# Optimization experiments

Measured on AMD Instinct MI355X. Metric: run time of the kernel, lower is better.

The kernel has to match this reference:

```python
import jax, jax.numpy as jnp
import numpy as np

B, D, H, E, C = 16384, 1024, 2048, 8, 3


def setup_inputs() -> dict:
    key = jax.random.key(0)
    ks = jax.random.split(key, 5)
    s_in = 1.0 / np.sqrt(D)
    s_h = 1.0 / np.sqrt(H)
    return {
        "x": jax.random.normal(ks[0], (B, D), dtype=jnp.float32),
        "Wr": jax.random.normal(ks[1], (D, E), dtype=jnp.float32) * s_in,
        "br": jnp.zeros((E,), dtype=jnp.float32),
        "W1": jax.random.normal(ks[2], (E, D, H), dtype=jnp.float32) * s_in,
        "b1": jnp.zeros((E, H), dtype=jnp.float32),
        "W2": jax.random.normal(ks[3], (E, H, C), dtype=jnp.float32) * s_h,
        "b2": jnp.zeros((E, C), dtype=jnp.float32),
    }


def reference(x, Wr, br, W1, b1, W2, b2):
    # Router: hard top-1 topic assignment per row.  [B]
    topics = jnp.argmax(x @ Wr + br, axis=1)
    # Dense dispatch: run every expert on all tokens (jit-friendly equivalent
    # of the masked per-expert loop), then combine by selecting the routed
    # expert's output per row.
    h = jax.nn.relu(jnp.einsum("bd,edh->ebh", x, W1) + b1[:, None, :])  # [E,B,H]
    out_all = jnp.einsum("ebh,ehc->ebc", h, W2) + b2[:, None, :]        # [E,B,C]
    preds = out_all[topics, jnp.arange(x.shape[0])]                     # [B,C]
    return preds
```

## Files before the change

kernel.cpp:

```cpp
#include <hip/hip_runtime.h>
#include <hip/hip_bf16.h>
#include <stdint.h>

#define NB 16384
#define ND 1024
#define NH 2048
#define NE 8
#define NC 3
#define MAXWL 136

typedef __attribute__((ext_vector_type(8))) short short8;
typedef __attribute__((ext_vector_type(4))) short short4v;
typedef __attribute__((ext_vector_type(4))) float f32x4;

__device__ __forceinline__ unsigned short f2bf(float f) {
  union { float f; unsigned int u; } v; v.f = f;
  unsigned int u = v.u;
  return (unsigned short)((u + 0x7fffu + ((u >> 16) & 1u)) >> 16);
}

__device__ __forceinline__ void glds16(const void* g, void* l) {
  __builtin_amdgcn_global_load_lds(
      (const __attribute__((address_space(1))) void*)g,
      (__attribute__((address_space(3))) void*)l,
      16, 0, 0);
}

__global__ __launch_bounds__(256) void router_kernel(
    const float* __restrict__ x, const float* __restrict__ Wr,
    const float* __restrict__ br, unsigned short* __restrict__ xb,
    int* __restrict__ topics) {
  int w = threadIdx.x >> 6, lane = threadIdx.x & 63;
  int row0 = blockIdx.x * 16 + w * 4;
  const float* xr[4];
  unsigned short* xbr[4];
#pragma unroll
  for (int r = 0; r < 4; ++r) {
    xr[r] = x + (size_t)(row0 + r) * ND;
    xbr[r] = xb + (size_t)(row0 + r) * ND;
  }
  f32x4 xv[4][4];
#pragma unroll
  for (int r = 0; r < 4; ++r)
#pragma unroll
    for (int i = 0; i < 4; ++i)
      xv[r][i] = *(const f32x4*)(xr[r] + i * 256 + lane * 4);
  float p[4][NE];
#pragma unroll
  for (int r = 0; r < 4; ++r)
#pragma unroll
    for (int e = 0; e < NE; ++e) p[r][e] = 0.f;
#pragma unroll
  for (int i = 0; i < 4; ++i) {
    int k0 = i * 256 + lane * 4;
#pragma unroll
    for (int r = 0; r < 4; ++r) {
      short4v s;
#pragma unroll
      for (int j = 0; j < 4; ++j) s[j] = (short)f2bf(xv[r][i][j]);
      *(short4v*)(xbr[r] + k0) = s;
    }
#pragma unroll
    for (int j = 0; j < 4; ++j) {
      const f32x4* wp = (const f32x4*)(Wr + (size_t)(k0 + j) * NE);
      f32x4 wa = wp[0], wb = wp[1];
#pragma unroll
      for (int r = 0; r < 4; ++r) {
        float a = xv[r][i][j];
        p[r][0] = fmaf(a, wa[0], p[r][0]);
        p[r][1] = fmaf(a, wa[1], p[r][1]);
        p[r][2] = fmaf(a, wa[2], p[r][2]);
        p[r][3] = fmaf(a, wa[3], p[r][3]);
        p[r][4] = fmaf(a, wb[0], p[r][4]);
        p[r][5] = fmaf(a, wb[1], p[r][5]);
        p[r][6] = fmaf(a, wb[2], p[r][6]);
        p[r][7] = fmaf(a, wb[3], p[r][7]);
      }
    }
  }
#pragma unroll
  for (int r = 0; r < 4; ++r)
#pragma unroll
    for (int e = 0; e < NE; ++e) {
#pragma unroll
      for (int d = 1; d < 64; d <<= 1) p[r][e] += __shfl_xor(p[r][e], d);
    }
  if (lane == 0) {
#pragma unroll
    for (int r = 0; r < 4; ++r) {
      float best = -1e30f;
      int bi = 0;
#pragma unroll
      for (int e = 0; e < NE; ++e) {
        float v = p[r][e] + br[e];
        if (v > best) { best = v; bi = e; }
      }
      topics[row0 + r] = bi;
    }
  }
}

__global__ __launch_bounds__(1024) void ranker_w1t_kernel(
    const int* __restrict__ topics, const float* __restrict__ W1,
    unsigned short* __restrict__ w1t, int* __restrict__ perm,
    int* __restrict__ counts, int* __restrict__ offsets,
    int* __restrict__ worklist, int* __restrict__ n_wl) {
  __shared__ __align__(16) char smem[8 * 64 * 67 * 2];
  __shared__ int soff[NE];
  int tid = threadIdx.x;

  if (blockIdx.x < 512) {
    unsigned short(*sbuf_t)[64][67] = (unsigned short(*)[64][67])smem;
    int bid = blockIdx.x;
    int e = bid >> 6;
    int rem = bid & 63;
    int kb = rem >> 2;
    int hb0 = (rem & 3) * 8;
    int kl = tid >> 4;
    int h0 = (tid & 15) * 4;
    const float* src = W1 + ((size_t)e * ND + kb * 64) * NH + hb0 * 64;
    f32x4 v[8];
#pragma unroll
    for (int q = 0; q < 8; ++q)
      v[q] = *(const f32x4*)(src + (size_t)kl * NH + q * 64 + h0);
#pragma unroll
    for (int q = 0; q < 8; ++q) {
#pragma unroll
      for (int j = 0; j < 4; ++j) sbuf_t[q][kl][h0 + j] = f2bf(v[q][j]);
    }
    __syncthreads();
#pragma unroll
    for (int s = 0; s < 4; ++s) {
      int flat = s * 1024 + tid;
      int q = flat >> 9;
      int idx = flat & 511;
      int hl = idx >> 3;
      int c8 = (idx & 7) * 8;
      short8 sv;
#pragma unroll
      for (int j = 0; j < 8; ++j) sv[j] = (short)sbuf_t[q][c8 + j][hl];
      unsigned short* dst =
          w1t + ((size_t)e * NH + (hb0 + q) * 64 + hl) * ND + kb * 64 + c8;
      *(short8*)dst = sv;
    }
    return;
  }

  uint4* sbuf = (uint4*)smem;
  int t[16];
  const int4* tp = (const int4*)(topics + tid * 16);
#pragma unroll
  for (int i = 0; i < 4; ++i) {
    int4 v = tp[i];
    t[i * 4 + 0] = v.x; t[i * 4 + 1] = v.y;
    t[i * 4 + 2] = v.z; t[i * 4 + 3] = v.w;
  }
  int h[NE] = {0, 0, 0, 0, 0, 0, 0, 0};
#pragma unroll
  for (int i = 0; i < 16; ++i) {
#pragma unroll
    for (int q = 0; q < NE; ++q) h[q] += (t[i] == q);
  }
  uint4 pk;
  pk.x = (unsigned)h[0] | ((unsigned)h[1] << 16);
  pk.y = (unsigned)h[2] | ((unsigned)h[3] << 16);
  pk.z = (unsigned)h[4] | ((unsigned)h[5] << 16);
  pk.w = (unsigned)h[6] | ((unsigned)h[7] << 16);
  uint4 own = pk;
  sbuf[tid] = pk;
  __syncthreads();
  for (int d = 1; d < 1024; d <<= 1) {
    uint4 v = {0u, 0u, 0u, 0u};
    if (tid >= d) v = sbuf[tid - d];
    __syncthreads();
    pk.x += v.x; pk.y += v.y; pk.z += v.z; pk.w += v.w;
    sbuf[tid] = pk;
    __syncthreads();
  }
  if (tid == 0) {
    uint4 tot = sbuf[1023];
    int c[NE] = {(int)(tot.x & 0xffff), (int)(tot.x >> 16),
                 (int)(tot.y & 0xffff), (int)(tot.y >> 16),
                 (int)(tot.z & 0xffff), (int)(tot.z >> 16),
                 (int)(tot.w & 0xffff), (int)(tot.w >> 16)};
    int s = 0, nw = 0;
    for (int e = 0; e < NE; ++e) {
      counts[e] = c[e];
      offsets[e] = s;
      soff[e] = s;
      s += c[e];
      for (int mt = 0; mt * 128 < c[e]; ++mt) worklist[nw++] = (e << 16) | mt;
    }
    *n_wl = nw;
  }
  __syncthreads();
  uint4 ex;
  ex.x = pk.x - own.x; ex.y = pk.y - own.y;
  ex.z = pk.z - own.z; ex.w = pk.w - own.w;
  int r[NE] = {soff[0] + (int)(ex.x & 0xffff), soff[1] + (int)(ex.x >> 16),
               soff[2] + (int)(ex.y & 0xffff), soff[3] + (int)(ex.y >> 16),
               soff[4] + (int)(ex.z & 0xffff), soff[5] + (int)(ex.z >> 16),
               soff[6] + (int)(ex.w & 0xffff), soff[7] + (int)(ex.w >> 16)};
#pragma unroll
  for (int i = 0; i < 16; ++i) {
    int e = t[i];
    int pos = 0;
#pragma unroll
    for (int q = 0; q < NE; ++q) pos = (e == q) ? r[q] : pos;
    perm[pos] = tid * 16 + i;
#pragma unroll
    for (int q = 0; q < NE; ++q) r[q] += (e == q);
  }
}

#define MF(a, b, c) __builtin_amdgcn_mfma_f32_16x16x32_bf16((a), (b), (c), 0, 0, 0)

#define STAGE(AS, BS, kt)                                         \
  do {                                                            \
    _Pragma("unroll") for (int i_ = 0; i_ < 4; ++i_) {            \
      glds16(aptr[i_] + (kt), (char*)(AS) + (i_ * 256 + t) * 16); \
      glds16(bptr[i_] + (kt), (char*)(BS) + (i_ * 256 + t) * 16); \
    }                                                             \
  } while (0)

#define PHASE(AS, BS, KT2)                                            \
  {                                                                   \
    short8 af_[2][4], bf_[2][4];                                      \
    _Pragma("unroll") for (int kk_ = 0; kk_ < 2; ++kk_) {             \
      int ch_ = ((kk_ * 4 + g) ^ sx) * 8;                             \
      _Pragma("unroll") for (int m_ = 0; m_ < 4; ++m_)                \
          af_[kk_][m_] = *(const short8*)&(AS)[arow + m_ * 1024 + ch_]; \
      _Pragma("unroll") for (int n_ = 0; n_ < 4; ++n_)                \
          bf_[kk_][n_] = *(const short8*)&(BS)[brow + n_ * 1024 + ch_]; \
    }                                                                 \
    __builtin_amdgcn_s_setprio(1);                                    \
    _Pragma("unroll") for (int kk_ = 0; kk_ < 2; ++kk_)               \
        _Pragma("unroll") for (int m_ = 0; m_ < 4; ++m_)              \
            _Pragma("unroll") for (int n_ = 0; n_ < 4; ++n_)          \
                acc[m_][n_] = MF(af_[kk_][m_], bf_[kk_][n_], acc[m_][n_]); \
    __builtin_amdgcn_s_setprio(0);                                    \
    asm volatile("s_waitcnt lgkmcnt(0)" ::: "memory");                \
    __builtin_amdgcn_s_barrier();                                     \
    STAGE(AS, BS, KT2);                                               \
    asm volatile("s_waitcnt vmcnt(8)" ::: "memory");                  \
    __builtin_amdgcn_s_barrier();                                     \
  }

__global__ __launch_bounds__(256, 2) void moe_gemm_kernel(
    const unsigned short* __restrict__ xb, const unsigned short* __restrict__ w1t,
    const float* __restrict__ b1, const float* __restrict__ W2,
    const int* __restrict__ perm, const int* __restrict__ counts,
    const int* __restrict__ offsets, const int* __restrict__ worklist,
    const int* __restrict__ n_wl, float* __restrict__ partial) {
  int nt = blockIdx.x & 15;
  int wi = blockIdx.x >> 4;
  if (wi >= *n_wl) return;
  int item = worklist[wi];
  int e = item >> 16;
  int mt = item & 0xffff;
  int cnt = counts[e];
  int off = offsets[e];
  int t = threadIdx.x;
  int lane = t & 63;
  int w = t >> 6, wr = w >> 1, wc = w & 1;

  __shared__ int ridx[128];
  __shared__ unsigned short As0[128 * 64];
  __shared__ unsigned short Bs0[128 * 64];
  __shared__ unsigned short As1[128 * 64];
  __shared__ unsigned short Bs1[128 * 64];

  if (t < 128) {
    int m = mt * 128 + t;
    ridx[t] = perm[off + (m < cnt ? m : cnt - 1)];
  }

  int cg = lane & 15;
  int g = lane >> 4;
  float b1v[4];
  float w2v[4][3];
#pragma unroll
  for (int n = 0; n < 4; ++n) {
    int col = nt * 128 + wc * 64 + n * 16 + cg;
    b1v[n] = b1[e * NH + col];
    const float* w2p = W2 + ((size_t)e * NH + col) * NC;
    w2v[n][0] = w2p[0];
    w2v[n][1] = w2p[1];
    w2v[n][2] = w2p[2];
  }
  asm volatile("" ::"v"(b1v[0]), "v"(b1v[1]), "v"(b1v[2]), "v"(b1v[3]),
               "v"(w2v[0][0]), "v"(w2v[0][1]), "v"(w2v[0][2]), "v"(w2v[1][0]),
               "v"(w2v[1][1]), "v"(w2v[1][2]), "v"(w2v[2][0]), "v"(w2v[2][1]),
               "v"(w2v[2][2]), "v"(w2v[3][0]), "v"(w2v[3][1]), "v"(w2v[3][2]));
  __syncthreads();

  const unsigned short* aptr[4];
  const unsigned short* bptr[4];
#pragma unroll
  for (int i = 0; i < 4; ++i) {
    int idx = i * 256 + t;
    int r = idx >> 3;
    int c = idx & 7;
    int cs = c ^ (r & 7);
    aptr[i] = xb + (size_t)ridx[r] * ND + cs * 8;
    bptr[i] = w1t + ((size_t)(e * NH + nt * 128 + r)) * ND + cs * 8;
  }

  f32x4 acc[4][4];
#pragma unroll
  for (int m = 0; m < 4; ++m)
#pragma unroll
    for (int n = 0; n < 4; ++n) acc[m][n] = (f32x4){0.f, 0.f, 0.f, 0.f};

  int arow = (wr * 64 + (lane & 15)) * 64;
  int brow = (wc * 64 + (lane & 15)) * 64;
  int sx = lane & 7;

  STAGE(As0, Bs0, 0);
  STAGE(As1, Bs1, 64);
  asm volatile("s_waitcnt vmcnt(8)" ::: "memory");
  __builtin_amdgcn_s_barrier();

#pragma unroll 1
  for (int it = 0; it < 8; ++it) {
    int kt2 = (it < 7 ? it + 1 : it) * 128;
    PHASE(As0, Bs0, kt2);
    PHASE(As1, Bs1, kt2 + 64);
  }
  asm volatile("s_waitcnt vmcnt(0)" ::: "memory");

  float* pbase = partial + (((size_t)(wi * 16 + nt)) * 2 + wc) * 128 * NC;
#pragma unroll
  for (int m = 0; m < 4; ++m) {
#pragma unroll
    for (int i = 0; i < 4; ++i) {
      float s0 = 0.f, s1 = 0.f, s2 = 0.f;
#pragma unroll
      for (int n = 0; n < 4; ++n) {
        float h = acc[m][n][i] + b1v[n];
        h = h > 0.f ? h : 0.f;
        s0 = fmaf(h, w2v[n][0], s0);
        s1 = fmaf(h, w2v[n][1], s1);
        s2 = fmaf(h, w2v[n][2], s2);
      }
#pragma unroll
      for (int d = 1; d < 16; d <<= 1) {
        s0 += __shfl_xor(s0, d);
        s1 += __shfl_xor(s1, d);
        s2 += __shfl_xor(s2, d);
      }
      if (cg == 0) {
        int rloc = wr * 64 + m * 16 + g * 4 + i;
        float* pp = pbase + rloc * NC;
        pp[0] = s0;
        pp[1] = s1;
        pp[2] = s2;
      }
    }
  }
}

__global__ __launch_bounds__(384) void reduce_kernel(
    const float* __restrict__ partial, const float* __restrict__ b2,
    const int* __restrict__ perm, const int* __restrict__ counts,
    const int* __restrict__ offsets, const int* __restrict__ worklist,
    const int* __restrict__ n_wl, float* __restrict__ out) {
  int wi = blockIdx.x;
  if (wi >= *n_wl) return;
  int item = worklist[wi];
  int e = item >> 16;
  int mt = item & 0xffff;
  int cnt = counts[e];
  int off = offsets[e];
  int j = threadIdx.x;
  int r = j / 3, c = j - r * 3;
  int m = mt * 128 + r;
  if (m >= cnt) return;
  const float* p = partial + (size_t)wi * 32 * 384 + j;
  float s = 0.f;
#pragma unroll
  for (int q = 0; q < 32; ++q) s += p[q * 384];
  int tok = perm[off + m];
  out[tok * NC + c] = b2[e * NC + c] + s;
}

extern "C" void kernel_launch(void* const* d_in, const int* in_sizes, int n_in,
                              void* d_out, int out_size, void* d_ws,
                              size_t ws_size, hipStream_t stream) {
  const float* x = (const float*)d_in[0];
  const float* Wr = (const float*)d_in[1];
  const float* br = (const float*)d_in[2];
  const float* W1 = (const float*)d_in[3];
  const float* b1 = (const float*)d_in[4];
  const float* W2 = (const float*)d_in[5];
  const float* b2 = (const float*)d_in[6];
  float* out = (float*)d_out;

  char* ws = (char*)d_ws;
  unsigned short* xb = (unsigned short*)ws;
  unsigned short* w1t = (unsigned short*)(ws + (size_t)33554432);
  int* topics = (int*)(ws + (size_t)67108864);
  int* perm = topics + NB;
  int* counts = perm + NB;
  int* offsets = counts + NE;
  int* worklist = offsets + NE;
  int* n_wl = worklist + 256;
  float* partial = (float*)(ws + (size_t)67108864 + 135168);

  router_kernel<<<NB / 16, 256, 0, stream>>>(x, Wr, br, xb, topics);
  ranker_w1t_kernel<<<513, 1024, 0, stream>>>(topics, W1, w1t, perm, counts,
                                              offsets, worklist, n_wl);
  moe_gemm_kernel<<<MAXWL * 16, 256, 0, stream>>>(xb, w1t, b1, W2, perm,
                                                  counts, offsets, worklist,
                                                  n_wl, partial);
  reduce_kernel<<<MAXWL, 384, 0, stream>>>(partial, b2, perm, counts, offsets,
                                           worklist, n_wl, out);
}
```

Measured before the change: 172.2 us.

## Replace double-buffered LDS pipeline with single-buffer loop and higher occupancy

Replaces the hand-pipelined two-stage LDS double buffer (prefetch next K tile while computing the current one, with setprio and partial vmcnt waits) with a simple single-buffer loop: load tile, sync, compute, sync. LDS per block is halved and launch bounds are raised from 2 to 3 blocks per CU, relying on more resident blocks to hide global-load latency instead of intra-block overlap. The register-pinning asm for bias and W2 values is also removed. This trades explicit copy/compute overlap for occupancy, and it adds two full barriers per K step with exposed load latency inside each block.

```diff
diff --git a/kernel.cpp b/kernel.cpp
--- a/kernel.cpp
+++ b/kernel.cpp
@@ -223,30 +223,22 @@
     }                                                             \
   } while (0)
 
-#define PHASE(AS, BS, KT2)                                            \
-  {                                                                   \
-    short8 af_[2][4], bf_[2][4];                                      \
+#define COMPUTE(AS, BS)                                               \
+  do {                                                                \
     _Pragma("unroll") for (int kk_ = 0; kk_ < 2; ++kk_) {             \
       int ch_ = ((kk_ * 4 + g) ^ sx) * 8;                             \
+      short8 af_[4], bf_[4];                                          \
       _Pragma("unroll") for (int m_ = 0; m_ < 4; ++m_)                \
-          af_[kk_][m_] = *(const short8*)&(AS)[arow + m_ * 1024 + ch_]; \
+          af_[m_] = *(const short8*)&(AS)[arow + m_ * 1024 + ch_];    \
       _Pragma("unroll") for (int n_ = 0; n_ < 4; ++n_)                \
-          bf_[kk_][n_] = *(const short8*)&(BS)[brow + n_ * 1024 + ch_]; \
+          bf_[n_] = *(const short8*)&(BS)[brow + n_ * 1024 + ch_];    \
+      _Pragma("unroll") for (int m_ = 0; m_ < 4; ++m_)                \
+          _Pragma("unroll") for (int n_ = 0; n_ < 4; ++n_)            \
+              acc[m_][n_] = MF(af_[m_], bf_[n_], acc[m_][n_]);        \
     }                                                                 \
-    __builtin_amdgcn_s_setprio(1);                                    \
-    _Pragma("unroll") for (int kk_ = 0; kk_ < 2; ++kk_)               \
-        _Pragma("unroll") for (int m_ = 0; m_ < 4; ++m_)              \
-            _Pragma("unroll") for (int n_ = 0; n_ < 4; ++n_)          \
-                acc[m_][n_] = MF(af_[kk_][m_], bf_[kk_][n_], acc[m_][n_]); \
-    __builtin_amdgcn_s_setprio(0);                                    \
-    asm volatile("s_waitcnt lgkmcnt(0)" ::: "memory");                \
-    __builtin_amdgcn_s_barrier();                                     \
-    STAGE(AS, BS, KT2);                                               \
-    asm volatile("s_waitcnt vmcnt(8)" ::: "memory");                  \
-    __builtin_amdgcn_s_barrier();                                     \
-  }
-
-__global__ __launch_bounds__(256, 2) void moe_gemm_kernel(
+  } while (0)
+
+__global__ __launch_bounds__(256, 3) void moe_gemm_kernel(
     const unsigned short* __restrict__ xb, const unsigned short* __restrict__ w1t,
     const float* __restrict__ b1, const float* __restrict__ W2,
     const int* __restrict__ perm, const int* __restrict__ counts,
@@ -265,10 +257,8 @@
   int w = t >> 6, wr = w >> 1, wc = w & 1;
 
   __shared__ int ridx[128];
-  __shared__ unsigned short As0[128 * 64];
-  __shared__ unsigned short Bs0[128 * 64];
-  __shared__ unsigned short As1[128 * 64];
-  __shared__ unsigned short Bs1[128 * 64];
+  __shared__ unsigned short As[128 * 64];
+  __shared__ unsigned short Bs[128 * 64];
 
   if (t < 128) {
     int m = mt * 128 + t;
@@ -288,10 +278,6 @@
     w2v[n][1] = w2p[1];
     w2v[n][2] = w2p[2];
   }
-  asm volatile("" ::"v"(b1v[0]), "v"(b1v[1]), "v"(b1v[2]), "v"(b1v[3]),
-               "v"(w2v[0][0]), "v"(w2v[0][1]), "v"(w2v[0][2]), "v"(w2v[1][0]),
-               "v"(w2v[1][1]), "v"(w2v[1][2]), "v"(w2v[2][0]), "v"(w2v[2][1]),
-               "v"(w2v[2][2]), "v"(w2v[3][0]), "v"(w2v[3][1]), "v"(w2v[3][2]));
   __syncthreads();
 
   const unsigned short* aptr[4];
@@ -312,22 +298,17 @@
 #pragma unroll
     for (int n = 0; n < 4; ++n) acc[m][n] = (f32x4){0.f, 0.f, 0.f, 0.f};
 
-  int arow = (wr * 64 + (lane & 15)) * 64;
-  int brow = (wc * 64 + (lane & 15)) * 64;
+  int arow = (wr * 64 + cg) * 64;
+  int brow = (wc * 64 + cg) * 64;
   int sx = lane & 7;
 
-  STAGE(As0, Bs0, 0);
-  STAGE(As1, Bs1, 64);
-  asm volatile("s_waitcnt vmcnt(8)" ::: "memory");
-  __builtin_amdgcn_s_barrier();
-
 #pragma unroll 1
-  for (int it = 0; it < 8; ++it) {
-    int kt2 = (it < 7 ? it + 1 : it) * 128;
-    PHASE(As0, Bs0, kt2);
-    PHASE(As1, Bs1, kt2 + 64);
-  }
-  asm volatile("s_waitcnt vmcnt(0)" ::: "memory");
+  for (int kt = 0; kt < ND; kt += 64) {
+    STAGE(As, Bs, kt);
+    __syncthreads();
+    COMPUTE(As, Bs);
+    __syncthreads();
+  }
 
   float* pbase = partial + (((size_t)(wi * 16 + nt)) * 2 + wc) * 128 * NC;
 #pragma unroll
```

New measurement: 154.3 us. 1.12x faster.
